# Optimization experiments

Hardware: AMD Instinct MI355X
Metric: run time of the kernel (lower is better)

Reference implementation:

```python
import jax, jax.numpy as jnp
import numpy as np
from jax import lax

B, N, H, D = 4, 384, 8, 5          # graphs, nodes/graph, heads, max multi-hop dist
NE, E_TOT, DH, L = 2048, 8192, 256, 10  # edges/graph, total real edges, d_hidden, curve samples
N_SPATIAL, N_EDGE_DIST = 64, 128


def _bn(x, g, b):
    # eval-mode BatchNorm1d (running_mean=0, running_var=1): affine only
    return x * g + b


def _conv1d(x, w):
    # x: [E, C, L], w: [O, I, 3], SAME padding, stride 1
    return lax.conv_general_dilated(x, w, (1,), 'SAME',
                                    dimension_numbers=('NCH', 'OIH', 'NCH'))


def setup_inputs() -> dict:
    key = jax.random.key(0)
    ks = iter(jax.random.split(key, 64))
    nrm = lambda shape, s=0.02: jax.random.normal(next(ks), shape, jnp.float32) * s
    std = 0.02 / np.sqrt(12.0)  # init_params with n_layer=12 for Linear weights
    inp = {}
    inp['attn_bias'] = jax.random.normal(next(ks), (B, N + 1, N + 1), jnp.float32)
    inp['spatial_pos'] = jax.random.randint(next(ks), (B, N, N), 0, N_SPATIAL)
    inp['d2_dist'] = jax.random.normal(next(ks), (B, N, N, 32), jnp.float32)
    inp['a3_dist'] = jax.random.normal(next(ks), (B, N, N, 32), jnp.float32)
    inp['edge_data'] = jax.random.normal(next(ks), (E_TOT, L, 7), jnp.float32)
    inp['edge_path'] = jax.random.randint(next(ks), (B, N, N, D), 0, NE + 1)
    inp['edge_padding_mask'] = jnp.zeros((B, NE), bool)  # all real edges
    inp['src'] = jax.random.randint(next(ks), (E_TOT,), 0, B * N)
    inp['dst'] = jax.random.randint(next(ks), (E_TOT,), 0, B * N)
    inp['node_data'] = jax.random.normal(next(ks), (B * N, DH), jnp.float32)
    # --- parameters ---
    inp['spatial_emb'] = nrm((N_SPATIAL, H)).at[0].set(0.0)  # padding_idx=0
    inp['t_virtual'] = nrm((1, H))
    inp['w_d2'] = nrm((H, 32), std); inp['b_d2'] = jnp.zeros((H,), jnp.float32)
    inp['w_a3'] = nrm((H, 32), std); inp['b_a3'] = jnp.zeros((H,), jnp.float32)
    inp['cw1'] = nrm((64, 7, 3), std);  inp['cg1'] = jnp.ones((64,));  inp['cb1'] = jnp.zeros((64,))
    inp['cw2'] = nrm((128, 64, 3), std); inp['cg2'] = jnp.ones((128,)); inp['cb2'] = jnp.zeros((128,))
    inp['cw3'] = nrm((256, 128, 3), std); inp['cg3'] = jnp.ones((256,)); inp['cb3'] = jnp.zeros((256,))
    inp['cw_out'] = nrm((H, 256), std)
    # _EdgeConv (UV-Net style): proj Linear(d_hidden->H), MLP(H->64->H), BN, GIN eps
    inp['wp'] = nrm((H, DH), std); inp['bp'] = jnp.zeros((H,))
    inp['w1'] = nrm((64, H), std); inp['b1'] = jnp.zeros((64,))
    inp['g1'] = jnp.ones((64,)); inp['bb1'] = jnp.zeros((64,))
    inp['w2'] = nrm((H, 64), std); inp['b2'] = jnp.zeros((H,))
    inp['g_out'] = jnp.ones((H,)); inp['bb_out'] = jnp.zeros((H,))
    inp['eps'] = jnp.zeros((), jnp.float32)
    inp['edge_dis_w'] = nrm((N_EDGE_DIST * H * H, 1))
    return inp


def reference(attn_bias, spatial_pos, d2_dist, a3_dist, edge_data, edge_path,
              edge_padding_mask, src, dst, node_data, spatial_emb, t_virtual,
              w_d2, b_d2, w_a3, b_a3, cw1, cg1, cb1, cw2, cg2, cb2, cw3, cg3, cb3,
              cw_out, wp, bp, w1, b1, g1, bb1, w2, b2, g_out, bb_out, eps, edge_dis_w):
    gab = jnp.repeat(attn_bias[:, None], H, axis=1)            # [B,H,N+1,N+1]
    spb = spatial_emb[spatial_pos]                              # [B,N,N,H]
    d2b = d2_dist @ w_d2.T + b_d2                               # [B,N,N,H]
    a3b = a3_dist @ w_a3.T + b_a3                               # [B,N,N,H]
    # CurveEncoder on per-edge curve samples
    x = jnp.transpose(edge_data, (0, 2, 1))                     # [E,7,L]
    x = jax.nn.leaky_relu(_bn(_conv1d(x, cw1), cg1[:, None], cb1[:, None]))
    x = jax.nn.leaky_relu(_bn(_conv1d(x, cw2), cg2[:, None], cb2[:, None]))
    x = jax.nn.leaky_relu(_bn(_conv1d(x, cw3), cg3[:, None], cb3[:, None]))
    ef = jnp.mean(x, axis=-1) @ cw_out.T                        # [E,H]
    # _EdgeConv: combine endpoint node features with edge features
    proj = node_data @ wp.T + bp                                # [B*N,H]
    h = (1.0 + eps) * ef + proj[src] + proj[dst]
    h = jax.nn.relu(_bn(h @ w1.T + b1, g1, bb1)) @ w2.T + b2
    edge_out = jax.nn.relu(_bn(h, g_out, bb_out))               # [E,H]
    # scatter real-edge features into padded table (row NE stays zero = padding)
    valid = (~edge_padding_mask).reshape(-1)                    # [B*NE]
    gidx = jnp.maximum(jnp.cumsum(valid) - 1, 0)
    vals = jnp.where(valid[:, None], edge_out[gidx], 0.0).reshape(B, NE, H)
    edge_feature = jnp.zeros((B, NE + 1, H), edge_out.dtype).at[:, :NE].set(vals)
    # gather along multi-hop paths, per-distance head mixing (bmm), normalize
    ep = edge_path.reshape(B, N * N * D)
    edge_input = jax.vmap(lambda f, p: f[p])(edge_feature, ep)  # [B,N*N*D,H]
    edge_input = edge_input.reshape(B, N, N, D, H)
    wdis = edge_dis_w.reshape(-1, H, H)[:D]                     # [D,H,H]
    edge_input = jnp.einsum('bijdh,dhk->bijdk', edge_input, wdis)
    sp = jnp.where(spatial_pos == 0, 1, spatial_pos)
    sp = jnp.where(sp > 1, sp - 1, sp)
    sp = jnp.clip(sp, 0, D)
    edge_bias = edge_input.sum(-2) / sp[..., None].astype(edge_input.dtype)
    inner = spb + d2b + a3b + edge_bias                         # [B,N,N,H]
    gab = gab.at[:, :, 1:, 1:].add(jnp.transpose(inner, (0, 3, 1, 2)))
    t = t_virtual.reshape(1, H, 1)
    gab = gab.at[:, :, 1:, 0].add(t)
    gab = gab.at[:, :, 0, :].add(t)
    return gab + attn_bias[:, None]
```

## Files before the change

### kernel.cpp

```cpp
#include <hip/hip_runtime.h>

#define NB    4
#define NNODE 384
#define NH    8
#define ND    5
#define NEDGE 2048
#define NEP1  2049
#define ETOT  8192
#define DHID  256
#define NP1   385
#define SQ1   (NP1*NP1)
#define NPOS  98304
#define NPOS2 (NPOS + 2)

typedef __attribute__((ext_vector_type(8)))  short short8;
typedef __attribute__((ext_vector_type(16))) float float16;

__device__ __forceinline__ unsigned short f2bf(float f) {
    union { float f; unsigned int u; } v; v.f = f;
    unsigned int u = v.u;
    return (unsigned short)((u + 0x7FFFu + ((u >> 16) & 1u)) >> 16);
}
__device__ __forceinline__ unsigned pkbf(float a, float b) {
    return (unsigned)f2bf(a) | ((unsigned)f2bf(b) << 16);
}
__device__ __forceinline__ short8 mk8(unsigned a, unsigned b, unsigned c, unsigned d) {
    union { unsigned u[4]; short8 s; } x; x.u[0]=a; x.u[1]=b; x.u[2]=c; x.u[3]=d; return x.s;
}
__device__ __forceinline__ float leaky(float v) { return v > 0.f ? v : 0.01f * v; }
__device__ __forceinline__ float16 zero16() {
    float16 z;
#pragma unroll
    for (int i = 0; i < 16; ++i) z[i] = 0.f;
    return z;
}

__global__ __launch_bounds__(256) void prep_kernel(
    const float* __restrict__ cw1, const float* __restrict__ cw2, const float* __restrict__ cw3,
    const float* __restrict__ cw_out,
    const float* __restrict__ node_data, const float* __restrict__ wp, const float* __restrict__ bp,
    unsigned short* __restrict__ W1f, unsigned short* __restrict__ W2f, unsigned short* __restrict__ W3f,
    unsigned short* __restrict__ Wof,
    float* __restrict__ proj, float* __restrict__ edge_feature)
{
    int gid = blockIdx.x * 256 + threadIdx.x;
    if (gid < 98304) {
        int j = gid & 7, lane = (gid >> 3) & 63, blk = gid >> 9;
        int ks = blk & 7, tp = (blk >> 3) % 3, mt = blk / 24;
        int oc = mt * 32 + (lane & 31);
        int ic = ks * 16 + (lane >> 5) * 8 + j;
        W3f[gid] = f2bf(cw3[(oc * 128 + ic) * 3 + tp]);
    } else if (gid < 122880) {
        int f = gid - 98304;
        int j = f & 7, lane = (f >> 3) & 63, blk = f >> 9;
        int ks = blk & 3, tp = (blk >> 2) % 3, mt = blk / 12;
        int oc = mt * 32 + (lane & 31);
        int ic = ks * 16 + (lane >> 5) * 8 + j;
        W2f[f] = f2bf(cw2[(oc * 64 + ic) * 3 + tp]);
    } else if (gid < 124928) {
        int f = gid - 122880;
        int j = f & 7, lane = (f >> 3) & 63, blk = f >> 9;
        int ks = blk & 1, mt = blk >> 1;
        int oc = mt * 32 + (lane & 31);
        int k = ks * 16 + (lane >> 5) * 8 + j;
        int tp = k >> 3, c = k & 7;
        float v = (tp < 3 && c < 7) ? cw1[oc * 21 + c * 3 + tp] : 0.f;
        W1f[f] = f2bf(v);
    } else if (gid < 137216) {
        int f = gid - 124928;
        int v = f >> 3, h = f & 7;
        const float* nd = node_data + (size_t)v * DHID;
        const float* ww = wp + h * DHID;
        float acc = bp[h];
#pragma unroll 4
        for (int c = 0; c < DHID; c += 4)
            acc += nd[c]*ww[c] + nd[c+1]*ww[c+1] + nd[c+2]*ww[c+2] + nd[c+3]*ww[c+3];
        proj[f] = acc;
    } else if (gid < 137248) {
        int f = gid - 137216;
        int b = f >> 3, h = f & 7;
        edge_feature[((size_t)b * NEP1 + NEDGE) * NH + h] = 0.f;
    } else if (gid < 145440) {
        int f = gid - 137248;
        int j = f & 7, lane = (f >> 3) & 63, g = f >> 9;
        int m = lane & 31;
        int k = g * 16 + (lane >> 5) * 8 + j;
        Wof[f] = (m < 8) ? f2bf(cw_out[m * 256 + k]) : (unsigned short)0;
    }
}

#define X0_GROWS 8
__global__ __launch_bounds__(256) void pack_kernel(
    const float* __restrict__ edge_data,
    unsigned short* __restrict__ X0buf, unsigned short* __restrict__ X1buf,
    unsigned short* __restrict__ X2buf)
{
    int gid = blockIdx.x * 256 + threadIdx.x;
    const int NX0 = (NPOS + 2 * X0_GROWS) * 8;
    if (gid < NX0) {
        int row = gid >> 3, ch = gid & 7;
        int pos = row - X0_GROWS;
        unsigned short v = 0;
        if (pos >= 0 && pos < NPOS && ch < 7) {
            int pm = pos % 12;
            if (pm >= 1 && pm <= 10)
                v = f2bf(edge_data[(size_t)(pos / 12) * 70 + (pm - 1) * 7 + ch]);
        }
        X0buf[gid] = v;
    } else if (gid < NX0 + 128) {
        int f = gid - NX0;
        int p = f >> 5, rest = f & 31;
        int row = (rest >> 4) ? (NPOS + 1) : 0, col = rest & 15;
        X1buf[((size_t)p * NPOS2 + row) * 16 + col] = 0;
    } else if (gid < NX0 + 128 + 256) {
        int f = gid - NX0 - 128;
        int p = f >> 5, rest = f & 31;
        int row = (rest >> 4) ? (NPOS + 1) : 0, col = rest & 15;
        X2buf[((size_t)p * NPOS2 + row) * 16 + col] = 0;
    }
}

__global__ __launch_bounds__(256, 4) void conv1_kernel(
    const unsigned short* __restrict__ X0, const unsigned short* __restrict__ W1f,
    const float* __restrict__ cg1, const float* __restrict__ cb1,
    unsigned short* __restrict__ X1)
{
    const int t = threadIdx.x, wv = t >> 6, lane = t & 63;
    const int q = lane >> 5, n = lane & 31;
    const int pos = blockIdx.x * 128 + wv * 32 + n;

    float16 acc0 = zero16(), acc1 = zero16();
#pragma unroll
    for (int ks = 0; ks < 2; ++ks) {
        short8 b  = *(const short8*)(X0 + (pos - 1 + 2 * ks + q) * 8);
        short8 a0 = *(const short8*)(W1f + ((0 * 2 + ks) * 64 + lane) * 8);
        short8 a1 = *(const short8*)(W1f + ((1 * 2 + ks) * 64 + lane) * 8);
        acc0 = __builtin_amdgcn_mfma_f32_32x32x16_bf16(a0, b, acc0, 0, 0, 0);
        acc1 = __builtin_amdgcn_mfma_f32_32x32x16_bf16(a1, b, acc1, 0, 0, 0);
    }
    int pm = pos % 12;
    bool valid = (pm != 0) && (pm != 11);
#pragma unroll
    for (int mt = 0; mt < 2; ++mt) {
        const float16& acc = mt ? acc1 : acc0;
#pragma unroll
        for (int r2 = 0; r2 < 4; ++r2) {
            int oc0 = mt * 32 + 8 * r2 + 4 * q;
            float4 g4 = *(const float4*)(cg1 + oc0);
            float4 b4 = *(const float4*)(cb1 + oc0);
            unsigned short uu[4];
            uu[0] = valid ? f2bf(leaky(acc[r2*4+0] * g4.x + b4.x)) : (unsigned short)0;
            uu[1] = valid ? f2bf(leaky(acc[r2*4+1] * g4.y + b4.y)) : (unsigned short)0;
            uu[2] = valid ? f2bf(leaky(acc[r2*4+2] * g4.z + b4.z)) : (unsigned short)0;
            uu[3] = valid ? f2bf(leaky(acc[r2*4+3] * g4.w + b4.w)) : (unsigned short)0;
            uint2 pk; pk.x = uu[0] | ((unsigned)uu[1] << 16); pk.y = uu[2] | ((unsigned)uu[3] << 16);
            *(uint2*)(void*)(X1 + ((size_t)(oc0 >> 4) * NPOS2 + pos + 1) * 16 + (oc0 & 15)) = pk;
        }
    }
}

__global__ __launch_bounds__(256, 2) void conv2_kernel(
    const unsigned short* __restrict__ X1, const unsigned short* __restrict__ W2f,
    const float* __restrict__ cg2, const float* __restrict__ cb2,
    unsigned short* __restrict__ X2)
{
    const int t = threadIdx.x, wv = t >> 6, lane = t & 63;
    const int q = lane >> 5, n = lane & 31;
    const int grp = wv >> 1, mp = wv & 1;
    const int pbase = blockIdx.x * 192 + grp * 96;

    float16 acc[2][3];
#pragma unroll
    for (int i = 0; i < 2; ++i)
#pragma unroll
        for (int nt = 0; nt < 3; ++nt) acc[i][nt] = zero16();

#pragma unroll
    for (int tp = 0; tp < 3; ++tp) {
#pragma unroll
        for (int ks = 0; ks < 4; ++ks) {
            short8 a0 = *(const short8*)(W2f + ((((mp*2+0) * 3 + tp) * 4 + ks) * 64 + lane) * 8);
            short8 a1 = *(const short8*)(W2f + ((((mp*2+1) * 3 + tp) * 4 + ks) * 64 + lane) * 8);
#pragma unroll
            for (int nt = 0; nt < 3; ++nt) {
                short8 b = *(const short8*)(X1 + ((size_t)ks * NPOS2 + pbase + nt*32 + n + tp) * 16 + q * 8);
                acc[0][nt] = __builtin_amdgcn_mfma_f32_32x32x16_bf16(a0, b, acc[0][nt], 0, 0, 0);
                acc[1][nt] = __builtin_amdgcn_mfma_f32_32x32x16_bf16(a1, b, acc[1][nt], 0, 0, 0);
            }
        }
    }
#pragma unroll
    for (int nt = 0; nt < 3; ++nt) {
        int pos = pbase + nt * 32 + n;
        int pm = pos % 12;
        bool valid = (pm != 0) && (pm != 11);
#pragma unroll
        for (int i = 0; i < 2; ++i) {
            int mt = mp * 2 + i;
#pragma unroll
            for (int r2 = 0; r2 < 4; ++r2) {
                int oc0 = mt * 32 + 8 * r2 + 4 * q;
                float4 g4 = *(const float4*)(cg2 + oc0);
                float4 b4 = *(const float4*)(cb2 + oc0);
                unsigned short uu[4];
                uu[0] = valid ? f2bf(leaky(acc[i][nt][r2*4+0] * g4.x + b4.x)) : (unsigned short)0;
                uu[1] = valid ? f2bf(leaky(acc[i][nt][r2*4+1] * g4.y + b4.y)) : (unsigned short)0;
                uu[2] = valid ? f2bf(leaky(acc[i][nt][r2*4+2] * g4.z + b4.z)) : (unsigned short)0;
                uu[3] = valid ? f2bf(leaky(acc[i][nt][r2*4+3] * g4.w + b4.w)) : (unsigned short)0;
                uint2 pk; pk.x = uu[0] | ((unsigned)uu[1] << 16); pk.y = uu[2] | ((unsigned)uu[3] << 16);
                *(uint2*)(void*)(X2 + ((size_t)(oc0 >> 4) * NPOS2 + pos + 1) * 16 + (oc0 & 15)) = pk;
            }
        }
    }
}

__global__ __launch_bounds__(256, 2) void conv3_kernel(
    const unsigned short* __restrict__ X2, const unsigned short* __restrict__ W3f,
    const unsigned short* __restrict__ Wof,
    const float* __restrict__ cg3, const float* __restrict__ cb3,
    const int* __restrict__ src, const int* __restrict__ dst,
    const float* __restrict__ w1, const float* __restrict__ b1,
    const float* __restrict__ g1, const float* __restrict__ bb1,
    const float* __restrict__ w2, const float* __restrict__ b2,
    const float* __restrict__ g_out, const float* __restrict__ bb_out,
    const float* __restrict__ eps, const float* __restrict__ proj,
    float* __restrict__ edge_feature)
{
    __shared__ float fs[3072 + 64 + 512];
    const int t = threadIdx.x, wv = t >> 6, lane = t & 63;
    const int q = lane >> 5, n = lane & 31;
    const int base = blockIdx.x * 96;

    float16 acc[2][3];
#pragma unroll
    for (int i = 0; i < 2; ++i)
#pragma unroll
        for (int nt = 0; nt < 3; ++nt) acc[i][nt] = zero16();

#pragma unroll
    for (int tp = 0; tp < 3; ++tp) {
#pragma unroll
        for (int ks = 0; ks < 8; ++ks) {
            short8 a0 = *(const short8*)(W3f + ((((wv*2+0) * 3 + tp) * 8 + ks) * 64 + lane) * 8);
            short8 a1 = *(const short8*)(W3f + ((((wv*2+1) * 3 + tp) * 8 + ks) * 64 + lane) * 8);
#pragma unroll
            for (int nt = 0; nt < 3; ++nt) {
                short8 b = *(const short8*)(X2 + ((size_t)ks * NPOS2 + base + nt*32 + n + tp) * 16 + q * 8);
                acc[0][nt] = __builtin_amdgcn_mfma_f32_32x32x16_bf16(a0, b, acc[0][nt], 0, 0, 0);
                acc[1][nt] = __builtin_amdgcn_mfma_f32_32x32x16_bf16(a1, b, acc[1][nt], 0, 0, 0);
            }
        }
    }

    short8 wof[4];
#pragma unroll
    for (int g = 0; g < 4; ++g)
        wof[g] = *(const short8*)(Wof + ((wv * 4 + g) * 64 + lane) * 8);

#pragma unroll
    for (int nt = 0; nt < 3; ++nt) {
        int pm = (nt * 32 + n) % 12;
        bool valid = (pm != 0) && (pm != 11);
        float16 p = zero16();
#pragma unroll
        for (int i = 0; i < 2; ++i) {
            int mt = wv * 2 + i;
            float av[16];
#pragma unroll
            for (int r2 = 0; r2 < 4; ++r2) {
                int oc0 = mt * 32 + 8 * r2 + 4 * q;
                float4 g4 = *(const float4*)(cg3 + oc0);
                float4 b4 = *(const float4*)(cb3 + oc0);
                av[r2*4+0] = valid ? leaky(acc[i][nt][r2*4+0] * g4.x + b4.x) : 0.f;
                av[r2*4+1] = valid ? leaky(acc[i][nt][r2*4+1] * g4.y + b4.y) : 0.f;
                av[r2*4+2] = valid ? leaky(acc[i][nt][r2*4+2] * g4.z + b4.z) : 0.f;
                av[r2*4+3] = valid ? leaky(acc[i][nt][r2*4+3] * g4.w + b4.w) : 0.f;
            }
            unsigned pk[8], op[8];
#pragma unroll
            for (int z = 0; z < 8; ++z) pk[z] = pkbf(av[2*z], av[2*z+1]);
#pragma unroll
            for (int z = 0; z < 8; ++z) op[z] = __shfl_xor((int)pk[z], 32);
            short8 f0 = q == 0 ? mk8(pk[0], pk[1], op[0], op[1])
                               : mk8(op[2], op[3], pk[2], pk[3]);
            short8 f1 = q == 0 ? mk8(pk[4], pk[5], op[4], op[5])
                               : mk8(op[6], op[7], pk[6], pk[7]);
            p = __builtin_amdgcn_mfma_f32_32x32x16_bf16(wof[i*2+0], f0, p, 0, 0, 0);
            p = __builtin_amdgcn_mfma_f32_32x32x16_bf16(wof[i*2+1], f1, p, 0, 0, 0);
        }
        float4 st = make_float4(p[0], p[1], p[2], p[3]);
        *(float4*)&fs[((wv * 96) + nt * 32 + n) * 8 + 4 * q] = st;
    }
    __syncthreads();

    if (t < 64) {
        int e = t >> 3, h = t & 7;
        float s = 0.f;
#pragma unroll
        for (int w = 0; w < 4; ++w)
#pragma unroll 4
            for (int l = 0; l < 12; ++l) s += fs[(w * 96 + e * 12 + l) * 8 + h];
        float efv = 0.1f * s;
        int ge = blockIdx.x * 8 + e;
        fs[3072 + e * 8 + h] = (1.f + eps[0]) * efv
                             + proj[src[ge] * NH + h] + proj[dst[ge] * NH + h];
    }
    __syncthreads();

#pragma unroll
    for (int bb = 0; bb < 512; bb += 256) {
        int idx = bb + t;
        int e = idx >> 6, o = idx & 63;
        float a = b1[o];
#pragma unroll
        for (int h = 0; h < 8; ++h) a += fs[3072 + e * 8 + h] * w1[o * 8 + h];
        float v = a * g1[o] + bb1[o];
        fs[3136 + e * 64 + o] = v > 0.f ? v : 0.f;
    }
    __syncthreads();

    if (t < 64) {
        int e = t >> 3, h = t & 7;
        float a = b2[h];
#pragma unroll 8
        for (int o = 0; o < 64; ++o) a += fs[3136 + e * 64 + o] * w2[h * 64 + o];
        float v = a * g_out[h] + bb_out[h];
        v = v > 0.f ? v : 0.f;
        int ge = blockIdx.x * 8 + e;
        int b = ge >> 11, el2 = ge & (NEDGE - 1);
        edge_feature[((size_t)b * NEP1 + el2) * NH + h] = v;
    }
}

__global__ __launch_bounds__(256) void bias_kernel(
    const float* __restrict__ attn_bias, const int* __restrict__ spatial_pos,
    const float* __restrict__ d2_dist, const float* __restrict__ a3_dist,
    const int* __restrict__ edge_path,
    const float* __restrict__ spatial_emb, const float* __restrict__ t_virtual,
    const float* __restrict__ w_d2, const float* __restrict__ b_d2,
    const float* __restrict__ w_a3, const float* __restrict__ b_a3,
    const float* __restrict__ edge_dis_w,
    const float* __restrict__ edge_feature,
    float* __restrict__ out)
{
    __shared__ __align__(16) float s_emb[512];
    __shared__ __align__(16) float s_wd2[256];
    __shared__ __align__(16) float s_wa3[256];
    __shared__ __align__(16) float s_wdis[320];
    __shared__ float s_t[8], s_bd2[8], s_ba3[8];

    int t = threadIdx.x;
    for (int i = t; i < 512; i += 256) s_emb[i] = spatial_emb[i];
    if (t < 256) { s_wd2[t] = w_d2[t]; s_wa3[t] = w_a3[t]; }
    for (int i = t; i < 320; i += 256) s_wdis[i] = edge_dis_w[i];
    if (t < 8) { s_t[t] = t_virtual[t]; s_bd2[t] = b_d2[t]; s_ba3[t] = b_a3[t]; }
    __syncthreads();

    int gc = blockIdx.x * 32 + (t >> 3);
    int part = t & 7;
    if (gc >= NB * SQ1) return;
    int b   = gc / SQ1;
    int rem = gc % SQ1;
    int i = rem / NP1, j = rem % NP1;

    float base = 2.f * attn_bias[gc];
    bool border = (i == 0) || (j == 0);
    int r = border ? 0 : i - 1, c = border ? 0 : j - 1;
    size_t nidx = ((size_t)b * NNODE + r) * NNODE + c;
    int sp = spatial_pos[nidx];

    float acc[8];
    {
        float4 vd = ((const float4*)(d2_dist + nidx * 32))[part];
        float4 va = ((const float4*)(a3_dist + nidx * 32))[part];
        const float4* wd2 = (const float4*)s_wd2;
        const float4* wa3 = (const float4*)s_wa3;
#pragma unroll
        for (int h = 0; h < 8; ++h) {
            float4 w4 = wd2[h * 8 + part];
            float4 v4 = wa3[h * 8 + part];
            acc[h] = vd.x*w4.x + vd.y*w4.y + vd.z*w4.z + vd.w*w4.w
                   + va.x*v4.x + va.y*v4.y + va.z*v4.z + va.w*v4.w;
        }
    }

    float ed[8] = {0,0,0,0,0,0,0,0};
    const int* ep = edge_path + nidx * ND;
    const float* efb = edge_feature + (size_t)b * NEP1 * NH;
#pragma unroll
    for (int d = 0; d < ND; ++d) {
        int pi = ep[d];
        float v = efb[(size_t)pi * NH + part];
        const float4* wr = (const float4*)(s_wdis + d * 64 + part * 8);
        float4 wa = wr[0], wb = wr[1];
        ed[0] += v*wa.x; ed[1] += v*wa.y; ed[2] += v*wa.z; ed[3] += v*wa.w;
        ed[4] += v*wb.x; ed[5] += v*wb.y; ed[6] += v*wb.z; ed[7] += v*wb.w;
    }
    int spd = (sp == 0) ? 1 : sp;
    spd = (spd > 1) ? spd - 1 : spd;
    spd = (spd > ND) ? ND : spd;
    float inv = 1.f / (float)spd;

    float rs[8];
#pragma unroll
    for (int h = 0; h < 8; ++h) rs[h] = acc[h] + ed[h] * inv;
#pragma unroll
    for (int m = 1; m < 8; m <<= 1) {
#pragma unroll
        for (int h = 0; h < 8; ++h) rs[h] += __shfl_xor(rs[h], m, 64);
    }

    float val = border ? (base + s_t[part])
                       : (base + rs[part] + s_emb[sp * 8 + part] + s_bd2[part] + s_ba3[part]);
    out[((size_t)b * NH + part) * SQ1 + (size_t)i * NP1 + j] = val;
}

extern "C" void kernel_launch(void* const* d_in, const int* in_sizes, int n_in,
                              void* d_out, int out_size, void* d_ws, size_t ws_size,
                              hipStream_t stream)
{
    const float* attn_bias   = (const float*)d_in[0];
    const int*   spatial_pos = (const int*)  d_in[1];
    const float* d2_dist     = (const float*)d_in[2];
    const float* a3_dist     = (const float*)d_in[3];
    const float* edge_data   = (const float*)d_in[4];
    const int*   edge_path   = (const int*)  d_in[5];
    const int*   src         = (const int*)  d_in[7];
    const int*   dst         = (const int*)  d_in[8];
    const float* node_data   = (const float*)d_in[9];
    const float* spatial_emb = (const float*)d_in[10];
    const float* t_virtual   = (const float*)d_in[11];
    const float* w_d2        = (const float*)d_in[12];
    const float* b_d2        = (const float*)d_in[13];
    const float* w_a3        = (const float*)d_in[14];
    const float* b_a3        = (const float*)d_in[15];
    const float* cw1         = (const float*)d_in[16];
    const float* cg1         = (const float*)d_in[17];
    const float* cb1         = (const float*)d_in[18];
    const float* cw2         = (const float*)d_in[19];
    const float* cg2         = (const float*)d_in[20];
    const float* cb2         = (const float*)d_in[21];
    const float* cw3         = (const float*)d_in[22];
    const float* cg3         = (const float*)d_in[23];
    const float* cb3         = (const float*)d_in[24];
    const float* cw_out      = (const float*)d_in[25];
    const float* wp          = (const float*)d_in[26];
    const float* bp          = (const float*)d_in[27];
    const float* w1          = (const float*)d_in[28];
    const float* b1          = (const float*)d_in[29];
    const float* g1          = (const float*)d_in[30];
    const float* bb1         = (const float*)d_in[31];
    const float* w2          = (const float*)d_in[32];
    const float* b2          = (const float*)d_in[33];
    const float* g_out       = (const float*)d_in[34];
    const float* bb_out      = (const float*)d_in[35];
    const float* eps         = (const float*)d_in[36];
    const float* edge_dis_w  = (const float*)d_in[37];

    float*          proj  = (float*)d_ws;
    float*          ef    = proj + NB * NNODE * NH;
    unsigned short* W1f   = (unsigned short*)(ef + NB * NEP1 * NH);
    unsigned short* W2f   = W1f + 2048;
    unsigned short* W3f   = W2f + 24576;
    unsigned short* Wof   = W3f + 98304;
    unsigned short* X0buf = Wof + 8192;
    unsigned short* X1buf = X0buf + (size_t)(NPOS + 2 * X0_GROWS) * 8;
    unsigned short* X2buf = X1buf + (size_t)4 * NPOS2 * 16;
    unsigned short* X0 = X0buf + X0_GROWS * 8;

    prep_kernel<<<569, 256, 0, stream>>>(cw1, cw2, cw3, cw_out, node_data, wp, bp,
                                         W1f, W2f, W3f, Wof, proj, ef);
    pack_kernel<<<3074, 256, 0, stream>>>(edge_data, X0buf, X1buf, X2buf);

    conv1_kernel<<<NPOS / 128, 256, 0, stream>>>(X0, W1f, cg1, cb1, X1buf);
    conv2_kernel<<<NPOS / 192, 256, 0, stream>>>(X1buf, W2f, cg2, cb2, X2buf);
    conv3_kernel<<<NPOS / 96, 256, 0, stream>>>(X2buf, W3f, Wof, cg3, cb3,
                                                src, dst, w1, b1, g1, bb1,
                                                w2, b2, g_out, bb_out, eps,
                                                proj, ef);

    int nbias = (NB * SQ1 * 8 + 255) / 256;
    bias_kernel<<<nbias, 256, 0, stream>>>(
        attn_bias, spatial_pos, d2_dist, a3_dist, edge_path,
        spatial_emb, t_virtual, w_d2, b_d2, w_a3, b_a3,
        edge_dis_w, ef, (float*)d_out);
}
```

Baseline: 365.3 us.

## Stage conv inputs in LDS via async loads and precompute edge-distance tables

conv2 and conv3 now stage the shared input tile in double-buffered LDS using global_load_lds, instead of having each wave reload overlapping positions from global memory. conv2 is retiled to 96 positions per block with one M-tile per wave, and its occupancy hint is raised to 3. A new tbl_kernel precomputes, per graph and distance, the edge features already mixed by the per-distance head weights. The bias kernel then does one gather per hop instead of an 8-wide multiply per hop. This adds a kernel launch and reuses the X0 workspace as the table buffer, and the syncthreads per K-step add barrier cost.

```diff
diff --git a/kernel.cpp b/kernel.cpp
--- a/kernel.cpp
+++ b/kernel.cpp
@@ -33,6 +33,12 @@
 #pragma unroll
     for (int i = 0; i < 16; ++i) z[i] = 0.f;
     return z;
+}
+__device__ __forceinline__ void gl_lds16(const void* g, void* l) {
+    __builtin_amdgcn_global_load_lds(
+        (const __attribute__((address_space(1))) unsigned int*)g,
+        (__attribute__((address_space(3))) unsigned int*)l,
+        16, 0, 0);
 }
 
 __global__ __launch_bounds__(256) void prep_kernel(
@@ -159,57 +165,61 @@
     }
 }
 
-__global__ __launch_bounds__(256, 2) void conv2_kernel(
+__global__ __launch_bounds__(256, 3) void conv2_kernel(
     const unsigned short* __restrict__ X1, const unsigned short* __restrict__ W2f,
     const float* __restrict__ cg2, const float* __restrict__ cb2,
     unsigned short* __restrict__ X2)
 {
+    __shared__ __align__(16) unsigned short sB[2][1568];
     const int t = threadIdx.x, wv = t >> 6, lane = t & 63;
     const int q = lane >> 5, n = lane & 31;
-    const int grp = wv >> 1, mp = wv & 1;
-    const int pbase = blockIdx.x * 192 + grp * 96;
-
-    float16 acc[2][3];
-#pragma unroll
-    for (int i = 0; i < 2; ++i)
-#pragma unroll
-        for (int nt = 0; nt < 3; ++nt) acc[i][nt] = zero16();
-
-#pragma unroll
-    for (int tp = 0; tp < 3; ++tp) {
-#pragma unroll
-        for (int ks = 0; ks < 4; ++ks) {
-            short8 a0 = *(const short8*)(W2f + ((((mp*2+0) * 3 + tp) * 4 + ks) * 64 + lane) * 8);
-            short8 a1 = *(const short8*)(W2f + ((((mp*2+1) * 3 + tp) * 4 + ks) * 64 + lane) * 8);
+    const int base = blockIdx.x * 96;
+    const int cbase = (wv < 3) ? wv * 64 : 132;
+
+    gl_lds16(X1 + ((size_t)0 * NPOS2 + base) * 16 + (cbase + lane) * 8,
+             &sB[0][cbase * 8]);
+
+    float16 acc[3];
+#pragma unroll
+    for (int nt = 0; nt < 3; ++nt) acc[nt] = zero16();
+
+    __syncthreads();
+
+#pragma unroll
+    for (int ks = 0; ks < 4; ++ks) {
+        if (ks < 3)
+            gl_lds16(X1 + ((size_t)(ks + 1) * NPOS2 + base) * 16 + (cbase + lane) * 8,
+                     &sB[(ks + 1) & 1][cbase * 8]);
+        const unsigned short* bb = sB[ks & 1];
+#pragma unroll
+        for (int tp = 0; tp < 3; ++tp) {
+            short8 a = *(const short8*)(W2f + (((wv * 3 + tp) * 4 + ks) * 64 + lane) * 8);
 #pragma unroll
             for (int nt = 0; nt < 3; ++nt) {
-                short8 b = *(const short8*)(X1 + ((size_t)ks * NPOS2 + pbase + nt*32 + n + tp) * 16 + q * 8);
-                acc[0][nt] = __builtin_amdgcn_mfma_f32_32x32x16_bf16(a0, b, acc[0][nt], 0, 0, 0);
-                acc[1][nt] = __builtin_amdgcn_mfma_f32_32x32x16_bf16(a1, b, acc[1][nt], 0, 0, 0);
+                short8 b = *(const short8*)(bb + (nt * 32 + n + tp) * 16 + q * 8);
+                acc[nt] = __builtin_amdgcn_mfma_f32_32x32x16_bf16(a, b, acc[nt], 0, 0, 0);
             }
         }
-    }
+        __syncthreads();
+    }
+
 #pragma unroll
     for (int nt = 0; nt < 3; ++nt) {
-        int pos = pbase + nt * 32 + n;
+        int pos = base + nt * 32 + n;
         int pm = pos % 12;
         bool valid = (pm != 0) && (pm != 11);
 #pragma unroll
-        for (int i = 0; i < 2; ++i) {
-            int mt = mp * 2 + i;
-#pragma unroll
-            for (int r2 = 0; r2 < 4; ++r2) {
-                int oc0 = mt * 32 + 8 * r2 + 4 * q;
-                float4 g4 = *(const float4*)(cg2 + oc0);
-                float4 b4 = *(const float4*)(cb2 + oc0);
-                unsigned short uu[4];
-                uu[0] = valid ? f2bf(leaky(acc[i][nt][r2*4+0] * g4.x + b4.x)) : (unsigned short)0;
-                uu[1] = valid ? f2bf(leaky(acc[i][nt][r2*4+1] * g4.y + b4.y)) : (unsigned short)0;
-                uu[2] = valid ? f2bf(leaky(acc[i][nt][r2*4+2] * g4.z + b4.z)) : (unsigned short)0;
-                uu[3] = valid ? f2bf(leaky(acc[i][nt][r2*4+3] * g4.w + b4.w)) : (unsigned short)0;
-                uint2 pk; pk.x = uu[0] | ((unsigned)uu[1] << 16); pk.y = uu[2] | ((unsigned)uu[3] << 16);
-                *(uint2*)(void*)(X2 + ((size_t)(oc0 >> 4) * NPOS2 + pos + 1) * 16 + (oc0 & 15)) = pk;
-            }
+        for (int r2 = 0; r2 < 4; ++r2) {
+            int oc0 = wv * 32 + 8 * r2 + 4 * q;
+            float4 g4 = *(const float4*)(cg2 + oc0);
+            float4 b4 = *(const float4*)(cb2 + oc0);
+            unsigned short uu[4];
+            uu[0] = valid ? f2bf(leaky(acc[nt][r2*4+0] * g4.x + b4.x)) : (unsigned short)0;
+            uu[1] = valid ? f2bf(leaky(acc[nt][r2*4+1] * g4.y + b4.y)) : (unsigned short)0;
+            uu[2] = valid ? f2bf(leaky(acc[nt][r2*4+2] * g4.z + b4.z)) : (unsigned short)0;
+            uu[3] = valid ? f2bf(leaky(acc[nt][r2*4+3] * g4.w + b4.w)) : (unsigned short)0;
+            uint2 pk; pk.x = uu[0] | ((unsigned)uu[1] << 16); pk.y = uu[2] | ((unsigned)uu[3] << 16);
+            *(uint2*)(void*)(X2 + ((size_t)(oc0 >> 4) * NPOS2 + pos + 1) * 16 + (oc0 & 15)) = pk;
         }
     }
 }
@@ -227,9 +237,14 @@
     float* __restrict__ edge_feature)
 {
     __shared__ float fs[3072 + 64 + 512];
+    __shared__ __align__(16) unsigned short sB[2][1568];
     const int t = threadIdx.x, wv = t >> 6, lane = t & 63;
     const int q = lane >> 5, n = lane & 31;
     const int base = blockIdx.x * 96;
+    const int cbase = (wv < 3) ? wv * 64 : 132;
+
+    gl_lds16(X2 + ((size_t)0 * NPOS2 + base) * 16 + (cbase + lane) * 8,
+             &sB[0][cbase * 8]);
 
     float16 acc[2][3];
 #pragma unroll
@@ -237,19 +252,26 @@
 #pragma unroll
         for (int nt = 0; nt < 3; ++nt) acc[i][nt] = zero16();
 
-#pragma unroll
-    for (int tp = 0; tp < 3; ++tp) {
-#pragma unroll
-        for (int ks = 0; ks < 8; ++ks) {
+    __syncthreads();
+
+#pragma unroll
+    for (int ks = 0; ks < 8; ++ks) {
+        if (ks < 7)
+            gl_lds16(X2 + ((size_t)(ks + 1) * NPOS2 + base) * 16 + (cbase + lane) * 8,
+                     &sB[(ks + 1) & 1][cbase * 8]);
+        const unsigned short* bb = sB[ks & 1];
+#pragma unroll
+        for (int tp = 0; tp < 3; ++tp) {
             short8 a0 = *(const short8*)(W3f + ((((wv*2+0) * 3 + tp) * 8 + ks) * 64 + lane) * 8);
             short8 a1 = *(const short8*)(W3f + ((((wv*2+1) * 3 + tp) * 8 + ks) * 64 + lane) * 8);
 #pragma unroll
             for (int nt = 0; nt < 3; ++nt) {
-                short8 b = *(const short8*)(X2 + ((size_t)ks * NPOS2 + base + nt*32 + n + tp) * 16 + q * 8);
+                short8 b = *(const short8*)(bb + (nt * 32 + n + tp) * 16 + q * 8);
                 acc[0][nt] = __builtin_amdgcn_mfma_f32_32x32x16_bf16(a0, b, acc[0][nt], 0, 0, 0);
                 acc[1][nt] = __builtin_amdgcn_mfma_f32_32x32x16_bf16(a1, b, acc[1][nt], 0, 0, 0);
             }
         }
+        __syncthreads();
     }
 
     short8 wof[4];
@@ -332,6 +354,22 @@
     }
 }
 
+__global__ __launch_bounds__(256) void tbl_kernel(
+    const float* __restrict__ edge_feature, const float* __restrict__ edge_dis_w,
+    float* __restrict__ T)
+{
+    int idx = blockIdx.x * 256 + threadIdx.x;
+    if (idx >= NEP1 * 8) return;
+    int pi = idx >> 3, k = idx & 7;
+    int d = blockIdx.y, b = blockIdx.z;
+    const float* ef = edge_feature + ((size_t)b * NEP1 + pi) * NH;
+    const float* w  = edge_dis_w + d * 64 + k;
+    float s = 0.f;
+#pragma unroll
+    for (int h = 0; h < 8; ++h) s += ef[h] * w[h * 8];
+    T[(((size_t)b * ND + d) * NEP1 + pi) * 8 + k] = s;
+}
+
 __global__ __launch_bounds__(256) void bias_kernel(
     const float* __restrict__ attn_bias, const int* __restrict__ spatial_pos,
     const float* __restrict__ d2_dist, const float* __restrict__ a3_dist,
@@ -339,20 +377,17 @@
     const float* __restrict__ spatial_emb, const float* __restrict__ t_virtual,
     const float* __restrict__ w_d2, const float* __restrict__ b_d2,
     const float* __restrict__ w_a3, const float* __restrict__ b_a3,
-    const float* __restrict__ edge_dis_w,
-    const float* __restrict__ edge_feature,
+    const float* __restrict__ Tbl,
     float* __restrict__ out)
 {
     __shared__ __align__(16) float s_emb[512];
     __shared__ __align__(16) float s_wd2[256];
     __shared__ __align__(16) float s_wa3[256];
-    __shared__ __align__(16) float s_wdis[320];
     __shared__ float s_t[8], s_bd2[8], s_ba3[8];
 
     int t = threadIdx.x;
     for (int i = t; i < 512; i += 256) s_emb[i] = spatial_emb[i];
     if (t < 256) { s_wd2[t] = w_d2[t]; s_wa3[t] = w_a3[t]; }
-    for (int i = t; i < 320; i += 256) s_wdis[i] = edge_dis_w[i];
     if (t < 8) { s_t[t] = t_virtual[t]; s_bd2[t] = b_d2[t]; s_ba3[t] = b_a3[t]; }
     __syncthreads();
 
@@ -384,34 +419,28 @@
         }
     }
 
-    float ed[8] = {0,0,0,0,0,0,0,0};
+    float edp = 0.f;
     const int* ep = edge_path + nidx * ND;
-    const float* efb = edge_feature + (size_t)b * NEP1 * NH;
+    const float* Tb = Tbl + (size_t)b * (ND * NEP1 * 8);
 #pragma unroll
     for (int d = 0; d < ND; ++d) {
         int pi = ep[d];
-        float v = efb[(size_t)pi * NH + part];
-        const float4* wr = (const float4*)(s_wdis + d * 64 + part * 8);
-        float4 wa = wr[0], wb = wr[1];
-        ed[0] += v*wa.x; ed[1] += v*wa.y; ed[2] += v*wa.z; ed[3] += v*wa.w;
-        ed[4] += v*wb.x; ed[5] += v*wb.y; ed[6] += v*wb.z; ed[7] += v*wb.w;
+        edp += Tb[((size_t)d * NEP1 + pi) * 8 + part];
     }
     int spd = (sp == 0) ? 1 : sp;
     spd = (spd > 1) ? spd - 1 : spd;
     spd = (spd > ND) ? ND : spd;
     float inv = 1.f / (float)spd;
 
-    float rs[8];
-#pragma unroll
-    for (int h = 0; h < 8; ++h) rs[h] = acc[h] + ed[h] * inv;
 #pragma unroll
     for (int m = 1; m < 8; m <<= 1) {
 #pragma unroll
-        for (int h = 0; h < 8; ++h) rs[h] += __shfl_xor(rs[h], m, 64);
+        for (int h = 0; h < 8; ++h) acc[h] += __shfl_xor(acc[h], m, 64);
     }
 
     float val = border ? (base + s_t[part])
-                       : (base + rs[part] + s_emb[sp * 8 + part] + s_bd2[part] + s_ba3[part]);
+                       : (base + acc[part] + edp * inv
+                          + s_emb[sp * 8 + part] + s_bd2[part] + s_ba3[part]);
     out[((size_t)b * NH + part) * SQ1 + (size_t)i * NP1 + j] = val;
 }
 
@@ -467,21 +496,25 @@
     unsigned short* X1buf = X0buf + (size_t)(NPOS + 2 * X0_GROWS) * 8;
     unsigned short* X2buf = X1buf + (size_t)4 * NPOS2 * 16;
     unsigned short* X0 = X0buf + X0_GROWS * 8;
+    float*          Tbl   = (float*)X0buf;
 
     prep_kernel<<<569, 256, 0, stream>>>(cw1, cw2, cw3, cw_out, node_data, wp, bp,
                                          W1f, W2f, W3f, Wof, proj, ef);
     pack_kernel<<<3074, 256, 0, stream>>>(edge_data, X0buf, X1buf, X2buf);
 
     conv1_kernel<<<NPOS / 128, 256, 0, stream>>>(X0, W1f, cg1, cb1, X1buf);
-    conv2_kernel<<<NPOS / 192, 256, 0, stream>>>(X1buf, W2f, cg2, cb2, X2buf);
+    conv2_kernel<<<NPOS / 96, 256, 0, stream>>>(X1buf, W2f, cg2, cb2, X2buf);
     conv3_kernel<<<NPOS / 96, 256, 0, stream>>>(X2buf, W3f, Wof, cg3, cb3,
                                                 src, dst, w1, b1, g1, bb1,
                                                 w2, b2, g_out, bb_out, eps,
                                                 proj, ef);
 
+    dim3 tgrid((NEP1 * 8 + 255) / 256, ND, NB);
+    tbl_kernel<<<tgrid, 256, 0, stream>>>(ef, edge_dis_w, Tbl);
+
     int nbias = (NB * SQ1 * 8 + 255) / 256;
     bias_kernel<<<nbias, 256, 0, stream>>>(
         attn_bias, spatial_pos, d2_dist, a3_dist, edge_path,
         spatial_emb, t_virtual, w_d2, b_d2, w_a3, b_a3,
-        edge_dis_w, ef, (float*)d_out);
-}
+        Tbl, (float*)d_out);
+}
```

New measurement: 355.6 us. 2.7% less time.
